# Kernel optimization log

Hardware: AMD Instinct MI355X
Metric: run time of the kernel (lower is better)

Reference implementation:

```python
import jax, jax.numpy as jnp
import numpy as np


def setup_inputs() -> dict:
    key = jax.random.key(0)
    k1, k2 = jax.random.split(key)
    B, C, h, w = 8, 128, 56, 56
    query_feature = jax.random.normal(k1, (B, C, h, w), dtype=jnp.float32)
    support_feature = jax.random.normal(k2, (B, C, h, w), dtype=jnp.float32)
    return {"query_feature": query_feature, "support_feature": support_feature}


def reference(query_feature, support_feature):
    q, s = query_feature, support_feature
    B, C, h, w = support_feature.shape
    N = h * w
    # torch .view semantics == row-major reshape (NOT a transpose)
    qf = jnp.reshape(query_feature, (B, N, C))      # [B, N, C]
    sf = jnp.reshape(support_feature, (B, C, N))    # [B, C, N]
    batch_adj = jnp.einsum('bnc,bcm->bnm', qf, sf)  # [B, N, N]
    attn = jax.nn.softmax(batch_adj, axis=-1)
    query_logits = jnp.einsum('bnm,bmc->bnc', attn, qf)          # [B, N, C]
    attention_mask = jax.nn.sigmoid(jnp.sum(batch_adj, axis=-1)) # [B, N]
    query_logits = query_logits * attention_mask[..., None]
    sf2 = jnp.reshape(support_feature, (B, N, C))   # another raw view
    support_logits = sf2 * attention_mask[..., None]
    query_logits = jnp.reshape(query_logits, (B, C, h, w))
    support_logits = jnp.reshape(support_logits, (B, C, h, w))
    return (q + query_logits, s + support_logits)
```

## Files before the change

kernel.cpp:

```cpp
#include <hip/hip_runtime.h>
#include <math.h>

#define B_ 8
#define C_ 128
#define N_ 3136
#define MT 64
#define TILES 49
#define QTBIG 128
#define QTILES 25

typedef short bf16x8 __attribute__((ext_vector_type(8)));
typedef float f32x4 __attribute__((ext_vector_type(4)));

__device__ __forceinline__ unsigned short f2bf(float f) {
    union { float f; unsigned u; } x; x.f = f;
    return (unsigned short)((x.u + 0x8000u) >> 16);
}

__device__ __forceinline__ void gl_lds16(const void* g, void* l) {
    __builtin_amdgcn_global_load_lds(
        (const __attribute__((address_space(1))) unsigned int*)g,
        (__attribute__((address_space(3))) unsigned int*)l, 16, 0, 0);
}

__global__ __launch_bounds__(256) void colsum_kernel(const float* __restrict__ s,
                                                     float* __restrict__ csum) {
    int blk = blockIdx.x;
    const float* p = s + (size_t)blk * N_;
    float acc = 0.f;
    for (int i = threadIdx.x; i < N_; i += 256) acc += p[i];
#pragma unroll
    for (int off = 32; off > 0; off >>= 1) acc += __shfl_down(acc, off, 64);
    __shared__ float part[4];
    if ((threadIdx.x & 63) == 0) part[threadIdx.x >> 6] = acc;
    __syncthreads();
    if (threadIdx.x == 0) csum[blk] = part[0] + part[1] + part[2] + part[3];
}

__global__ __launch_bounds__(256) void prep_kernel(const float* __restrict__ q,
                                                   const float* __restrict__ s,
                                                   unsigned short* __restrict__ sfT,
                                                   unsigned short* __restrict__ qfT,
                                                   float* __restrict__ csum) {
    __shared__ unsigned short T[8448];
    const int tid = threadIdx.x, bid = blockIdx.x;
    const int b = bid & 7, m0 = (bid >> 3) * 64;
    const float* sb = s + (size_t)b * C_ * N_;
    const float* qb = q + (size_t)b * C_ * N_;

    unsigned short (*TA)[132] = (unsigned short (*)[132])T;
#pragma unroll
    for (int st = 0; st < 8; ++st) {
        int idx = st * 256 + tid;
        int c = idx >> 4, m4 = (idx & 15) * 4;
        float4 v = *(const float4*)&sb[(size_t)c * N_ + m0 + m4];
        TA[m4 + 0][c] = f2bf(v.x);
        TA[m4 + 1][c] = f2bf(v.y);
        TA[m4 + 2][c] = f2bf(v.z);
        TA[m4 + 3][c] = f2bf(v.w);
        float ps = (v.x + v.y) + (v.z + v.w);
        ps += __shfl_xor(ps, 1, 16);
        ps += __shfl_xor(ps, 2, 16);
        ps += __shfl_xor(ps, 4, 16);
        ps += __shfl_xor(ps, 8, 16);
        if ((tid & 15) == 0) atomicAdd(&csum[b * C_ + c], ps);
    }
    __syncthreads();
    {
        unsigned short* dst = sfT + (size_t)b * N_ * C_;
#pragma unroll
        for (int st = 0; st < 4; ++st) {
            int g = st * 256 + tid;
            int mr = g >> 4, p = g & 15;
            int sw = (mr & 15) ^ ((mr >> 1) & 4);
            int lch = p ^ sw;
            const unsigned short* src = &TA[mr][lch * 8];
            ushort4 a = *(const ushort4*)src;
            ushort4 bq = *(const ushort4*)(src + 4);
            uint4 w;
            w.x = a.x | ((unsigned)a.y << 16);   w.y = a.z | ((unsigned)a.w << 16);
            w.z = bq.x | ((unsigned)bq.y << 16); w.w = bq.z | ((unsigned)bq.w << 16);
            *(uint4*)&dst[(size_t)(m0 + mr) * C_ + p * 8] = w;
        }
    }
    __syncthreads();

    unsigned short (*TB)[66] = (unsigned short (*)[66])T;
#pragma unroll
    for (int st = 0; st < 8; ++st) {
        int idx = st * 256 + tid;
        int r = idx >> 5, c4 = (idx & 31) * 4;
        float4 v = *(const float4*)&qb[(size_t)(m0 + r) * C_ + c4];
        TB[c4 + 0][r] = f2bf(v.x);
        TB[c4 + 1][r] = f2bf(v.y);
        TB[c4 + 2][r] = f2bf(v.z);
        TB[c4 + 3][r] = f2bf(v.w);
    }
    __syncthreads();
    {
        unsigned short* dstb = qfT + (size_t)b * N_ * C_;
#pragma unroll
        for (int st = 0; st < 4; ++st) {
            int g = st * 256 + tid;
            int p = g >> 7, c = g & 127;
            const unsigned short* src = &TB[c][p * 8];
            ushort2 a0 = *(const ushort2*)(src);
            ushort2 a1 = *(const ushort2*)(src + 2);
            ushort2 a2 = *(const ushort2*)(src + 4);
            ushort2 a3 = *(const ushort2*)(src + 6);
            uint4 w;
            w.x = a0.x | ((unsigned)a0.y << 16); w.y = a1.x | ((unsigned)a1.y << 16);
            w.z = a2.x | ((unsigned)a2.y << 16); w.w = a3.x | ((unsigned)a3.y << 16);
            *(uint4*)&dstb[((size_t)(m0 >> 6) * 8 + p) * (C_ * 8) + c * 8] = w;
        }
    }
}

__global__ __launch_bounds__(512, 1) void fused_full_kernel(
    const float* __restrict__ q, const float* __restrict__ s,
    const float* __restrict__ csum,
    const unsigned short* __restrict__ sfT,
    const unsigned short* __restrict__ qfT,
    float* __restrict__ out0, float* __restrict__ out1) {

    __shared__ __align__(16) unsigned char SM[QTBIG * 132 * 4];
    __shared__ float dred[2][QTBIG];
    __shared__ float mskd[QTBIG];
    __shared__ float cs[C_];

    unsigned short* Kb = (unsigned short*)SM;
    unsigned short* Vb = (unsigned short*)(SM + 32768);
    float (*Of)[132] = (float (*)[132])SM;

    const int tid = threadIdx.x;
    const int lane = tid & 63;
    const int wave = tid >> 6;
    const int l15 = lane & 15;
    const int quad = lane >> 4;
    const int qs = wave >> 1;
    const int mg = wave & 1;
    const int bid = blockIdx.x;
    const int b = bid & 7;
    const int qt = bid >> 3;
    const int n0 = qt * QTBIG;

    const float* qb = q + (size_t)b * C_ * N_;
    const unsigned short* sfTb = sfT + (size_t)b * N_ * C_;
    const unsigned short* qfTb = qfT + (size_t)b * N_ * C_;

    const int sig_base = ((l15 >> 2) << 3) + (l15 & 3);

    if (tid < C_) cs[tid] = csum[b * C_ + tid];

#pragma unroll
    for (int st = 0; st < 2; ++st) {
        int i = st * 512 + tid;
        gl_lds16(sfTb + (size_t)(i >> 4) * C_ + (i & 15) * 8,
                 &Kb[(st * 512 + wave * 64) * 8]);
        gl_lds16(qfTb + (size_t)i * 8,
                 &Vb[(st * 512 + wave * 64) * 8]);
    }
    __syncthreads();

    bf16x8 qa[2][4];
    float dotp[2];
#pragma unroll
    for (int rt = 0; rt < 2; ++rt) {
        int grow = n0 + qs * 32 + rt * 16 + l15;
        if (grow > N_ - 1) grow = N_ - 1;
        float dp = 0.f;
#pragma unroll
        for (int ks = 0; ks < 4; ++ks) {
            int c0 = ks * 32 + quad * 8;
            float4 f0 = *(const float4*)&qb[(size_t)grow * C_ + c0];
            float4 f1 = *(const float4*)&qb[(size_t)grow * C_ + c0 + 4];
            dp += f0.x * cs[c0 + 0] + f0.y * cs[c0 + 1] +
                  f0.z * cs[c0 + 2] + f0.w * cs[c0 + 3] +
                  f1.x * cs[c0 + 4] + f1.y * cs[c0 + 5] +
                  f1.z * cs[c0 + 6] + f1.w * cs[c0 + 7];
            union { unsigned short u[8]; bf16x8 v; } t;
            t.u[0] = f2bf(f0.x); t.u[1] = f2bf(f0.y);
            t.u[2] = f2bf(f0.z); t.u[3] = f2bf(f0.w);
            t.u[4] = f2bf(f1.x); t.u[5] = f2bf(f1.y);
            t.u[6] = f2bf(f1.z); t.u[7] = f2bf(f1.w);
            qa[rt][ks] = t.v;
        }
        dotp[rt] = dp;
    }
#pragma unroll
    for (int rt = 0; rt < 2; ++rt) {
        float d = dotp[rt];
        d += __shfl_xor(d, 16, 64);
        d += __shfl_xor(d, 32, 64);
        if (mg == 0 && quad == 0) mskd[qs * 32 + rt * 16 + l15] = d;
    }

    f32x4 O[2][8];
#pragma unroll
    for (int rt = 0; rt < 2; ++rt)
#pragma unroll
        for (int nt = 0; nt < 8; ++nt) O[rt][nt] = (f32x4){0.f, 0.f, 0.f, 0.f};
    float dsum[2] = {0.f, 0.f};

    for (int tt = 0; tt < TILES; ++tt) {
        const int cur = tt & 1;
        __syncthreads();

        if (tt + 1 < TILES) {
            const int nxt = cur ^ 1;
            const size_t m1 = (size_t)(tt + 1) * MT;
#pragma unroll
            for (int st = 0; st < 2; ++st) {
                int i = st * 512 + tid;
                gl_lds16(sfTb + (m1 + (i >> 4)) * C_ + (i & 15) * 8,
                         &Kb[nxt * (MT * C_) + (st * 512 + wave * 64) * 8]);
                gl_lds16(qfTb + (size_t)(tt + 1) * (MT * C_) + (size_t)i * 8,
                         &Vb[nxt * (MT * C_) + (st * 512 + wave * 64) * 8]);
            }
        }

        f32x4 acc[2][2];
        __builtin_amdgcn_s_setprio(1);
#pragma unroll
        for (int ct = 0; ct < 2; ++ct) {
            const int mrow = sig_base + (ct << 2);
            const int sw = (mrow & 15) ^ ((mrow >> 1) & 4);
            const int row = mg * 32 + mrow;
            acc[ct][0] = (f32x4){0.f, 0.f, 0.f, 0.f};
            acc[ct][1] = (f32x4){0.f, 0.f, 0.f, 0.f};
#pragma unroll
            for (int ks = 0; ks < 4; ++ks) {
                int ch = (ks * 4 + quad) ^ sw;
                bf16x8 af = *(const bf16x8*)&Kb[cur * (MT * C_) + row * C_ + ch * 8];
                acc[ct][0] = __builtin_amdgcn_mfma_f32_16x16x32_bf16(af, qa[0][ks], acc[ct][0], 0, 0, 0);
                acc[ct][1] = __builtin_amdgcn_mfma_f32_16x16x32_bf16(af, qa[1][ks], acc[ct][1], 0, 0, 0);
            }
        }
        __builtin_amdgcn_s_setprio(0);

        bf16x8 pa[2];
#pragma unroll
        for (int rt = 0; rt < 2; ++rt) {
            float e0 = __expf(acc[0][rt][0]);
            float e1 = __expf(acc[0][rt][1]);
            float e2 = __expf(acc[0][rt][2]);
            float e3 = __expf(acc[0][rt][3]);
            float e4 = __expf(acc[1][rt][0]);
            float e5 = __expf(acc[1][rt][1]);
            float e6 = __expf(acc[1][rt][2]);
            float e7 = __expf(acc[1][rt][3]);
            dsum[rt] += ((e0 + e1) + (e2 + e3)) + ((e4 + e5) + (e6 + e7));
            union { unsigned short u[8]; bf16x8 v; } pk;
            pk.u[0] = f2bf(e0); pk.u[1] = f2bf(e1);
            pk.u[2] = f2bf(e2); pk.u[3] = f2bf(e3);
            pk.u[4] = f2bf(e4); pk.u[5] = f2bf(e5);
            pk.u[6] = f2bf(e6); pk.u[7] = f2bf(e7);
            pa[rt] = pk.v;
        }

        __builtin_amdgcn_s_setprio(1);
#pragma unroll
        for (int nt = 0; nt < 8; ++nt) {
            bf16x8 vf = *(const bf16x8*)&Vb[cur * (MT * C_) + ((mg * 4 + quad) * C_ + nt * 16 + l15) * 8];
            O[0][nt] = __builtin_amdgcn_mfma_f32_16x16x32_bf16(pa[0], vf, O[0][nt], 0, 0, 0);
            O[1][nt] = __builtin_amdgcn_mfma_f32_16x16x32_bf16(pa[1], vf, O[1][nt], 0, 0, 0);
        }
        __builtin_amdgcn_s_setprio(0);
    }

#pragma unroll
    for (int rt = 0; rt < 2; ++rt) {
        float d = dsum[rt];
        d += __shfl_xor(d, 16, 64);
        d += __shfl_xor(d, 32, 64);
        if (quad == 0) dred[mg][qs * 32 + rt * 16 + l15] = d;
    }

    __syncthreads();

    if (mg == 1) {
#pragma unroll
        for (int rt = 0; rt < 2; ++rt)
#pragma unroll
            for (int nt = 0; nt < 8; ++nt)
#pragma unroll
                for (int r = 0; r < 4; ++r)
                    Of[qs * 32 + rt * 16 + quad * 4 + r][nt * 16 + l15] = O[rt][nt][r];
    }
    __syncthreads();
    if (mg == 0) {
#pragma unroll
        for (int rt = 0; rt < 2; ++rt)
#pragma unroll
            for (int nt = 0; nt < 8; ++nt)
#pragma unroll
                for (int r = 0; r < 4; ++r)
                    Of[qs * 32 + rt * 16 + quad * 4 + r][nt * 16 + l15] += O[rt][nt][r];
    }
    __syncthreads();

    const size_t vbase = (size_t)b * N_ * C_ + (size_t)n0 * C_;
#pragma unroll
    for (int it = 0; it < 8; ++it) {
        int row = it * 16 + (tid >> 5);
        int grow = n0 + row;
        if (grow >= N_) continue;
        int c = (tid & 31) * 4;
        float dt = dred[0][row] + dred[1][row];
        float mk = 1.0f / (1.0f + __expf(-mskd[row]));
        float scl = mk / dt;
        float om = 1.0f + mk;
        float4 o4 = *(const float4*)&Of[row][c];
        float4 q4 = *(const float4*)&q[vbase + (size_t)row * C_ + c];
        float4 s4 = *(const float4*)&s[vbase + (size_t)row * C_ + c];
        float4 r0v, r1v;
        r0v.x = q4.x + o4.x * scl;
        r0v.y = q4.y + o4.y * scl;
        r0v.z = q4.z + o4.z * scl;
        r0v.w = q4.w + o4.w * scl;
        r1v.x = s4.x * om; r1v.y = s4.y * om;
        r1v.z = s4.z * om; r1v.w = s4.w * om;
        *(float4*)&out0[vbase + (size_t)row * C_ + c] = r0v;
        *(float4*)&out1[vbase + (size_t)row * C_ + c] = r1v;
    }
}

__global__ __launch_bounds__(256, 2) void fused_kernel(const float* __restrict__ q,
                                                       const float* __restrict__ s,
                                                       const float* __restrict__ csum,
                                                       float* __restrict__ out0,
                                                       float* __restrict__ out1) {
    __shared__ float QtT[C_][68];
    __shared__ float Kt[C_ * 32];
    __shared__ float Vt[32 * C_];
    __shared__ float PT[32][68];
    __shared__ float mask_l[64];
    __shared__ float csum_l[C_];

    const int t = threadIdx.x;
    const int l = t & 63, w = t >> 6, tx = t & 15, ty = t >> 4;
    const int bid = blockIdx.x, b = bid & 7, n0 = (bid >> 3) * 64;
    const float* qb = q + (size_t)b * C_ * N_;
    const float* sb = s + (size_t)b * C_ * N_;

#pragma unroll
    for (int jj = 0; jj < 2; ++jj) {
        int c = l + 64 * jj;
#pragma unroll
        for (int i = 0; i < 16; ++i) QtT[c][w + 4 * i] = qb[(size_t)(n0 + w + 4 * i) * C_ + c];
    }
    if (t < C_) csum_l[t] = csum[b * C_ + t];
    __syncthreads();
    if (t < 64) {
        float d = 0.f;
        for (int c = 0; c < C_; ++c) d += QtT[c][t] * csum_l[c];
        mask_l[t] = 1.0f / (1.0f + __expf(-d));
    }
    float4 Oa[4], Ob[4];
#pragma unroll
    for (int i = 0; i < 4; ++i) { Oa[i] = make_float4(0,0,0,0); Ob[i] = make_float4(0,0,0,0); }
    float m_r[4], l_r[4];
#pragma unroll
    for (int i = 0; i < 4; ++i) { m_r[i] = -3.0e38f; l_r[i] = 0.f; }

    for (int mt = 0; mt < N_ / 32; ++mt) {
        const int m0 = mt * 32;
        __syncthreads();
#pragma unroll
        for (int i = 0; i < 4; ++i) {
            int s4 = (w * 4 + i) * 64 + l;
            int c = s4 >> 3, mq = (s4 & 7) * 4;
            *(float4*)&Kt[c * 32 + mq] = *(const float4*)&sb[(size_t)c * N_ + m0 + mq];
            *(float4*)&Vt[s4 * 4] = *(const float4*)&qb[(size_t)m0 * C_ + s4 * 4];
        }
        __syncthreads();
        float a[4][2];
#pragma unroll
        for (int i = 0; i < 4; ++i) a[i][0] = a[i][1] = 0.f;
#pragma unroll 4
        for (int k = 0; k < C_; ++k) {
            const float4 qv = *(const float4*)&QtT[k][4 * ty];
            const float2 kv = *(const float2*)&Kt[k * 32 + 2 * tx];
            a[0][0] = fmaf(qv.x, kv.x, a[0][0]); a[0][1] = fmaf(qv.x, kv.y, a[0][1]);
            a[1][0] = fmaf(qv.y, kv.x, a[1][0]); a[1][1] = fmaf(qv.y, kv.y, a[1][1]);
            a[2][0] = fmaf(qv.z, kv.x, a[2][0]); a[2][1] = fmaf(qv.z, kv.y, a[2][1]);
            a[3][0] = fmaf(qv.w, kv.x, a[3][0]); a[3][1] = fmaf(qv.w, kv.y, a[3][1]);
        }
#pragma unroll
        for (int i = 0; i < 4; ++i) {
            float tm = fmaxf(a[i][0], a[i][1]);
            tm = fmaxf(tm, __shfl_xor(tm, 1, 64)); tm = fmaxf(tm, __shfl_xor(tm, 2, 64));
            tm = fmaxf(tm, __shfl_xor(tm, 4, 64)); tm = fmaxf(tm, __shfl_xor(tm, 8, 64));
            float nm = fmaxf(m_r[i], tm);
            float al = __expf(m_r[i] - nm);
            m_r[i] = nm;
            float p0 = __expf(a[i][0] - nm), p1 = __expf(a[i][1] - nm);
            float ts = p0 + p1;
            ts += __shfl_xor(ts, 1, 64); ts += __shfl_xor(ts, 2, 64);
            ts += __shfl_xor(ts, 4, 64); ts += __shfl_xor(ts, 8, 64);
            l_r[i] = l_r[i] * al + ts;
            PT[2 * tx + 0][4 * ty + i] = p0;
            PT[2 * tx + 1][4 * ty + i] = p1;
            Oa[i].x *= al; Oa[i].y *= al; Oa[i].z *= al; Oa[i].w *= al;
            Ob[i].x *= al; Ob[i].y *= al; Ob[i].z *= al; Ob[i].w *= al;
        }
        __syncthreads();
#pragma unroll 2
        for (int j = 0; j < 32; ++j) {
            const float4 pv = *(const float4*)&PT[j][4 * ty];
            const float4 v0 = *(const float4*)&Vt[j * C_ + 4 * tx];
            const float4 v1 = *(const float4*)&Vt[j * C_ + 4 * tx + 64];
            Oa[0].x = fmaf(pv.x, v0.x, Oa[0].x); Oa[0].y = fmaf(pv.x, v0.y, Oa[0].y);
            Oa[0].z = fmaf(pv.x, v0.z, Oa[0].z); Oa[0].w = fmaf(pv.x, v0.w, Oa[0].w);
            Ob[0].x = fmaf(pv.x, v1.x, Ob[0].x); Ob[0].y = fmaf(pv.x, v1.y, Ob[0].y);
            Ob[0].z = fmaf(pv.x, v1.z, Ob[0].z); Ob[0].w = fmaf(pv.x, v1.w, Ob[0].w);
            Oa[1].x = fmaf(pv.y, v0.x, Oa[1].x); Oa[1].y = fmaf(pv.y, v0.y, Oa[1].y);
            Oa[1].z = fmaf(pv.y, v0.z, Oa[1].z); Oa[1].w = fmaf(pv.y, v0.w, Oa[1].w);
            Ob[1].x = fmaf(pv.y, v1.x, Ob[1].x); Ob[1].y = fmaf(pv.y, v1.y, Ob[1].y);
            Ob[1].z = fmaf(pv.y, v1.z, Ob[1].z); Ob[1].w = fmaf(pv.y, v1.w, Ob[1].w);
            Oa[2].x = fmaf(pv.z, v0.x, Oa[2].x); Oa[2].y = fmaf(pv.z, v0.y, Oa[2].y);
            Oa[2].z = fmaf(pv.z, v0.z, Oa[2].z); Oa[2].w = fmaf(pv.z, v0.w, Oa[2].w);
            Ob[2].x = fmaf(pv.z, v1.x, Ob[2].x); Ob[2].y = fmaf(pv.z, v1.y, Ob[2].y);
            Ob[2].z = fmaf(pv.z, v1.z, Ob[2].z); Ob[2].w = fmaf(pv.z, v1.w, Ob[2].w);
            Oa[3].x = fmaf(pv.w, v0.x, Oa[3].x); Oa[3].y = fmaf(pv.w, v0.y, Oa[3].y);
            Oa[3].z = fmaf(pv.w, v0.z, Oa[3].z); Oa[3].w = fmaf(pv.w, v0.w, Oa[3].w);
            Ob[3].x = fmaf(pv.w, v1.x, Ob[3].x); Ob[3].y = fmaf(pv.w, v1.y, Ob[3].y);
            Ob[3].z = fmaf(pv.w, v1.z, Ob[3].z); Ob[3].w = fmaf(pv.w, v1.w, Ob[3].w);
        }
    }
#pragma unroll
    for (int i = 0; i < 4; ++i) {
        const int r = 4 * ty + i;
        const float mk = mask_l[r];
        const float scl = mk / l_r[i];
        const float om = 1.0f + mk;
        const size_t row = (size_t)b * C_ * N_ + (size_t)(n0 + r) * C_;
#pragma unroll
        for (int h = 0; h < 2; ++h) {
            const int c = 4 * tx + 64 * h;
            const float4 ov = h ? Ob[i] : Oa[i];
            float4 qv = *(const float4*)&qb[(size_t)(n0 + r) * C_ + c];
            float4 sv = *(const float4*)&sb[(size_t)(n0 + r) * C_ + c];
            float4 o0, o1;
            o0.x = qv.x + ov.x * scl; o0.y = qv.y + ov.y * scl;
            o0.z = qv.z + ov.z * scl; o0.w = qv.w + ov.w * scl;
            o1.x = sv.x * om; o1.y = sv.y * om; o1.z = sv.z * om; o1.w = sv.w * om;
            *(float4*)&out0[row + c] = o0;
            *(float4*)&out1[row + c] = o1;
        }
    }
}

extern "C" void kernel_launch(void* const* d_in, const int* in_sizes, int n_in,
                              void* d_out, int out_size, void* d_ws, size_t ws_size,
                              hipStream_t stream) {
    const float* q = (const float*)d_in[0];
    const float* s = (const float*)d_in[1];
    float* out0 = (float*)d_out;
    float* out1 = out0 + (size_t)B_ * C_ * N_;
    float* csum = (float*)d_ws;

    const size_t elems = (size_t)B_ * N_ * C_;
    const size_t need = 4096
                      + 2 * elems * sizeof(unsigned short);

    if (ws_size >= need) {
        unsigned short* sfT = (unsigned short*)((char*)d_ws + 4096);
        unsigned short* qfT = sfT + elems;
        hipMemsetAsync(csum, 0, B_ * C_ * sizeof(float), stream);
        prep_kernel<<<B_ * TILES, 256, 0, stream>>>(q, s, sfT, qfT, csum);
        fused_full_kernel<<<QTILES * B_, 512, 0, stream>>>(q, s, csum, sfT, qfT, out0, out1);
    } else {
        colsum_kernel<<<B_ * C_, 256, 0, stream>>>(s, csum);
        fused_kernel<<<B_ * (N_ / 64), 256, 0, stream>>>(q, s, csum, out0, out1);
    }
}
```

Measured before the change: 162.2 us.

## Replace csum atomics with partial slices, split prep finer, pipeline K/V loads

The prep kernel now handles 32-column slices (twice as many blocks) and writes per-slice column partial sums to a strided buffer instead of using atomics. This removes the memset launch and the atomic contention, and the fused kernel reduces the 98 partials itself. The main loop swaps __syncthreads for explicit barriers with vmcnt waits so the next tile's global-to-LDS prefetch stays in flight, and it loads V fragments into registers before the QK MFMAs. bf16 packing uses the hardware v_cvt_pk_bf16_f32 instruction in place of manual rounding. Risks are higher register pressure from holding vfr, and possible hazards if the vmcnt(4) count does not match the number of outstanding loads.

New measurement: 152.6 us. 1.06x faster.

```diff
diff --git a/kernel.cpp b/kernel.cpp
--- a/kernel.cpp
+++ b/kernel.cpp
@@ -6,8 +6,10 @@
 #define N_ 3136
 #define MT 64
 #define TILES 49
+#define SLICES 98
 #define QTBIG 128
 #define QTILES 25
+#define CS_STRIDE 100
 
 typedef short bf16x8 __attribute__((ext_vector_type(8)));
 typedef float f32x4 __attribute__((ext_vector_type(4)));
@@ -15,6 +17,12 @@
 __device__ __forceinline__ unsigned short f2bf(float f) {
     union { float f; unsigned u; } x; x.f = f;
     return (unsigned short)((x.u + 0x8000u) >> 16);
+}
+
+__device__ __forceinline__ unsigned cvtpk(float lo, float hi) {
+    unsigned r;
+    asm("v_cvt_pk_bf16_f32 %0, %1, %2" : "=v"(r) : "v"(lo), "v"(hi));
+    return r;
 }
 
 __device__ __forceinline__ void gl_lds16(const void* g, void* l) {
@@ -41,35 +49,35 @@
                                                    const float* __restrict__ s,
                                                    unsigned short* __restrict__ sfT,
                                                    unsigned short* __restrict__ qfT,
-                                                   float* __restrict__ csum) {
-    __shared__ unsigned short T[8448];
+                                                   float* __restrict__ csump) {
+    __shared__ unsigned short T[4608];
     const int tid = threadIdx.x, bid = blockIdx.x;
-    const int b = bid & 7, m0 = (bid >> 3) * 64;
+    const int b = bid & 7, m0 = (bid >> 3) * 32;
+    const int slice = bid >> 3;
     const float* sb = s + (size_t)b * C_ * N_;
     const float* qb = q + (size_t)b * C_ * N_;
 
     unsigned short (*TA)[132] = (unsigned short (*)[132])T;
 #pragma unroll
-    for (int st = 0; st < 8; ++st) {
+    for (int st = 0; st < 4; ++st) {
         int idx = st * 256 + tid;
-        int c = idx >> 4, m4 = (idx & 15) * 4;
+        int c = idx >> 3, m4 = (idx & 7) * 4;
         float4 v = *(const float4*)&sb[(size_t)c * N_ + m0 + m4];
         TA[m4 + 0][c] = f2bf(v.x);
         TA[m4 + 1][c] = f2bf(v.y);
         TA[m4 + 2][c] = f2bf(v.z);
         TA[m4 + 3][c] = f2bf(v.w);
         float ps = (v.x + v.y) + (v.z + v.w);
-        ps += __shfl_xor(ps, 1, 16);
-        ps += __shfl_xor(ps, 2, 16);
-        ps += __shfl_xor(ps, 4, 16);
-        ps += __shfl_xor(ps, 8, 16);
-        if ((tid & 15) == 0) atomicAdd(&csum[b * C_ + c], ps);
+        ps += __shfl_xor(ps, 1, 8);
+        ps += __shfl_xor(ps, 2, 8);
+        ps += __shfl_xor(ps, 4, 8);
+        if ((tid & 7) == 0) csump[((size_t)b * C_ + c) * CS_STRIDE + slice] = ps;
     }
     __syncthreads();
     {
         unsigned short* dst = sfT + (size_t)b * N_ * C_;
 #pragma unroll
-        for (int st = 0; st < 4; ++st) {
+        for (int st = 0; st < 2; ++st) {
             int g = st * 256 + tid;
             int mr = g >> 4, p = g & 15;
             int sw = (mr & 15) ^ ((mr >> 1) & 4);
@@ -85,9 +93,9 @@
     }
     __syncthreads();
 
-    unsigned short (*TB)[66] = (unsigned short (*)[66])T;
-#pragma unroll
-    for (int st = 0; st < 8; ++st) {
+    unsigned short (*TB)[34] = (unsigned short (*)[34])T;
+#pragma unroll
+    for (int st = 0; st < 4; ++st) {
         int idx = st * 256 + tid;
         int r = idx >> 5, c4 = (idx & 31) * 4;
         float4 v = *(const float4*)&qb[(size_t)(m0 + r) * C_ + c4];
@@ -99,11 +107,12 @@
     __syncthreads();
     {
         unsigned short* dstb = qfT + (size_t)b * N_ * C_;
-#pragma unroll
-        for (int st = 0; st < 4; ++st) {
+        const int tile = m0 >> 6, pbase = (m0 & 32) >> 3;
+#pragma unroll
+        for (int st = 0; st < 2; ++st) {
             int g = st * 256 + tid;
-            int p = g >> 7, c = g & 127;
-            const unsigned short* src = &TB[c][p * 8];
+            int pl = g >> 7, c = g & 127;
+            const unsigned short* src = &TB[c][pl * 8];
             ushort2 a0 = *(const ushort2*)(src);
             ushort2 a1 = *(const ushort2*)(src + 2);
             ushort2 a2 = *(const ushort2*)(src + 4);
@@ -111,14 +120,14 @@
             uint4 w;
             w.x = a0.x | ((unsigned)a0.y << 16); w.y = a1.x | ((unsigned)a1.y << 16);
             w.z = a2.x | ((unsigned)a2.y << 16); w.w = a3.x | ((unsigned)a3.y << 16);
-            *(uint4*)&dstb[((size_t)(m0 >> 6) * 8 + p) * (C_ * 8) + c * 8] = w;
+            *(uint4*)&dstb[((size_t)tile * 8 + pbase + pl) * (C_ * 8) + c * 8] = w;
         }
     }
 }
 
 __global__ __launch_bounds__(512, 1) void fused_full_kernel(
     const float* __restrict__ q, const float* __restrict__ s,
-    const float* __restrict__ csum,
+    const float* __restrict__ csump,
     const unsigned short* __restrict__ sfT,
     const unsigned short* __restrict__ qfT,
     float* __restrict__ out0, float* __restrict__ out1) {
@@ -150,8 +159,6 @@
 
     const int sig_base = ((l15 >> 2) << 3) + (l15 & 3);
 
-    if (tid < C_) cs[tid] = csum[b * C_ + tid];
-
 #pragma unroll
     for (int st = 0; st < 2; ++st) {
         int i = st * 512 + tid;
@@ -159,6 +166,14 @@
                  &Kb[(st * 512 + wave * 64) * 8]);
         gl_lds16(qfTb + (size_t)i * 8,
                  &Vb[(st * 512 + wave * 64) * 8]);
+    }
+
+    if (tid < C_) {
+        float a = 0.f;
+        const float* cp = csump + ((size_t)b * C_ + tid) * CS_STRIDE;
+#pragma unroll 7
+        for (int sl = 0; sl < SLICES; ++sl) a += cp[sl];
+        cs[tid] = a;
     }
     __syncthreads();
 
@@ -178,11 +193,9 @@
                   f0.z * cs[c0 + 2] + f0.w * cs[c0 + 3] +
                   f1.x * cs[c0 + 4] + f1.y * cs[c0 + 5] +
                   f1.z * cs[c0 + 6] + f1.w * cs[c0 + 7];
-            union { unsigned short u[8]; bf16x8 v; } t;
-            t.u[0] = f2bf(f0.x); t.u[1] = f2bf(f0.y);
-            t.u[2] = f2bf(f0.z); t.u[3] = f2bf(f0.w);
-            t.u[4] = f2bf(f1.x); t.u[5] = f2bf(f1.y);
-            t.u[6] = f2bf(f1.z); t.u[7] = f2bf(f1.w);
+            union { unsigned w[4]; bf16x8 v; } t;
+            t.w[0] = cvtpk(f0.x, f0.y); t.w[1] = cvtpk(f0.z, f0.w);
+            t.w[2] = cvtpk(f1.x, f1.y); t.w[3] = cvtpk(f1.z, f1.w);
             qa[rt][ks] = t.v;
         }
         dotp[rt] = dp;
@@ -204,7 +217,8 @@
 
     for (int tt = 0; tt < TILES; ++tt) {
         const int cur = tt & 1;
-        __syncthreads();
+
+        __builtin_amdgcn_s_barrier();
 
         if (tt + 1 < TILES) {
             const int nxt = cur ^ 1;
@@ -217,7 +231,16 @@
                 gl_lds16(qfTb + (size_t)(tt + 1) * (MT * C_) + (size_t)i * 8,
                          &Vb[nxt * (MT * C_) + (st * 512 + wave * 64) * 8]);
             }
-        }
+            asm volatile("s_waitcnt vmcnt(4)" ::: "memory");
+        } else {
+            asm volatile("s_waitcnt vmcnt(0)" ::: "memory");
+        }
+        __builtin_amdgcn_s_barrier();
+
+        bf16x8 vfr[8];
+#pragma unroll
+        for (int nt = 0; nt < 8; ++nt)
+            vfr[nt] = *(const bf16x8*)&Vb[cur * (MT * C_) + ((mg * 4 + quad) * C_ + nt * 16 + l15) * 8];
 
         f32x4 acc[2][2];
         __builtin_amdgcn_s_setprio(1);
@@ -250,20 +273,17 @@
             float e6 = __expf(acc[1][rt][2]);
             float e7 = __expf(acc[1][rt][3]);
             dsum[rt] += ((e0 + e1) + (e2 + e3)) + ((e4 + e5) + (e6 + e7));
-            union { unsigned short u[8]; bf16x8 v; } pk;
-            pk.u[0] = f2bf(e0); pk.u[1] = f2bf(e1);
-            pk.u[2] = f2bf(e2); pk.u[3] = f2bf(e3);
-            pk.u[4] = f2bf(e4); pk.u[5] = f2bf(e5);
-            pk.u[6] = f2bf(e6); pk.u[7] = f2bf(e7);
+            union { unsigned w[4]; bf16x8 v; } pk;
+            pk.w[0] = cvtpk(e0, e1); pk.w[1] = cvtpk(e2, e3);
+            pk.w[2] = cvtpk(e4, e5); pk.w[3] = cvtpk(e6, e7);
             pa[rt] = pk.v;
         }
 
         __builtin_amdgcn_s_setprio(1);
 #pragma unroll
         for (int nt = 0; nt < 8; ++nt) {
-            bf16x8 vf = *(const bf16x8*)&Vb[cur * (MT * C_) + ((mg * 4 + quad) * C_ + nt * 16 + l15) * 8];
-            O[0][nt] = __builtin_amdgcn_mfma_f32_16x16x32_bf16(pa[0], vf, O[0][nt], 0, 0, 0);
-            O[1][nt] = __builtin_amdgcn_mfma_f32_16x16x32_bf16(pa[1], vf, O[1][nt], 0, 0, 0);
+            O[0][nt] = __builtin_amdgcn_mfma_f32_16x16x32_bf16(pa[0], vfr[nt], O[0][nt], 0, 0, 0);
+            O[1][nt] = __builtin_amdgcn_mfma_f32_16x16x32_bf16(pa[1], vfr[nt], O[1][nt], 0, 0, 0);
         }
         __builtin_amdgcn_s_setprio(0);
     }
@@ -458,19 +478,20 @@
     const float* s = (const float*)d_in[1];
     float* out0 = (float*)d_out;
     float* out1 = out0 + (size_t)B_ * C_ * N_;
-    float* csum = (float*)d_ws;
 
     const size_t elems = (size_t)B_ * N_ * C_;
-    const size_t need = 4096
+    const size_t csump_sz = (size_t)B_ * C_ * CS_STRIDE;
+    const size_t need = csump_sz * sizeof(float)
                       + 2 * elems * sizeof(unsigned short);
 
     if (ws_size >= need) {
-        unsigned short* sfT = (unsigned short*)((char*)d_ws + 4096);
+        float* csump = (float*)d_ws;
+        unsigned short* sfT = (unsigned short*)(csump + csump_sz);
         unsigned short* qfT = sfT + elems;
-        hipMemsetAsync(csum, 0, B_ * C_ * sizeof(float), stream);
-        prep_kernel<<<B_ * TILES, 256, 0, stream>>>(q, s, sfT, qfT, csum);
-        fused_full_kernel<<<QTILES * B_, 512, 0, stream>>>(q, s, csum, sfT, qfT, out0, out1);
+        prep_kernel<<<B_ * SLICES, 256, 0, stream>>>(q, s, sfT, qfT, csump);
+        fused_full_kernel<<<QTILES * B_, 512, 0, stream>>>(q, s, csump, sfT, qfT, out0, out1);
     } else {
+        float* csum = (float*)d_ws;
         colsum_kernel<<<B_ * C_, 256, 0, stream>>>(s, csum);
         fused_kernel<<<B_ * (N_ / 64), 256, 0, stream>>>(q, s, csum, out0, out1);
     }
```
